# Optimization experiments

Measured on AMD Instinct MI355X. Metric: run time of the kernel, lower is better.

The kernel has to match this reference:

```python
import jax, jax.numpy as jnp
import numpy as np

NS = 8  # number of bins (init arg ns)


def setup_inputs() -> dict:
    key = jax.random.key(0)
    x = jax.random.normal(key, (16, 512, 128, 128), dtype=jnp.float32)
    return {"x": x}


def _make_hk(Hc, C, ns, height):
    """Sequential threshold binning: per batch row, scan j and record bin edges.

    Hc: [B, height] exclusive cumulative counts of per-(b,c) argmax rows.
    Returns hks: [B, ns+1] float32 with hks[:,0]=0, hks[:,ns]=height.
    """

    def row_fn(hrow):
        hks0 = jnp.zeros(ns + 1, jnp.float32).at[ns].set(float(height))

        def step(carry, j):
            k, hks = carry
            t = ((k * C) // ns).astype(hrow.dtype)  # int(k*C/ns)
            cond = (k < ns) & (hrow[j] <= t) & (hrow[j + 1] > t)
            hks = hks.at[k].set(jnp.where(cond, j.astype(jnp.float32), hks[k]))
            k = k + cond.astype(k.dtype)
            return (k, hks), None

        # original loop: j in [1, height-2] (breaks when j+1 >= height)
        js = jnp.arange(1, height - 1, dtype=jnp.int32)
        (_, hks), _ = jax.lax.scan(step, (jnp.int32(1), hks0), js)
        return hks

    return jax.vmap(row_fn)(Hc)


def _forward(x, ns):
    B, C, H, W = x.shape
    a = x.reshape(B, C, H * W)
    vmax = jnp.max(a, axis=2, keepdims=True)
    # argmax indicator mask (ties all set to 1, matching a == max)
    I = (a == vmax).astype(x.dtype).reshape(B, C, H, W)
    # per-row counts of argmax positions, summed over channels & width: [B, H]
    rc = I.sum(axis=(1, 3))
    # H[:, i] = sum of I over rows < i  -> exclusive cumulative sum
    Hc = jnp.concatenate(
        [jnp.zeros((B, 1), x.dtype), jnp.cumsum(rc, axis=1)[:, :-1]], axis=1
    )
    hk = _make_hk(Hc, C, ns, H)  # [B, ns+1]
    F = x.sum(axis=(2, 3)) / W  # [B, C]
    hk_sub = hk[:, 1:] - hk[:, :-1]  # [B, ns]
    # F repeated over ns bins, divided by bin widths, flattened: [B, ns*C]
    return (F[:, None, :] / hk_sub[:, :, None]).reshape(B, ns * C)


def reference(x):
    return _forward(x, NS)
```

## Files before the change

### kernel.cpp

```cpp
#include <hip/hip_runtime.h>

#define Bdim 16
#define Cdim 512
#define Hdim 128
#define Wdim 128
#define NS 8

__global__ __launch_bounds__(256) void chan_reduce(const float* __restrict__ x,
                                                   int* __restrict__ rc,
                                                   float* __restrict__ F) {
    const int bid = blockIdx.x;
    const int tid = threadIdx.x;
    const float4* __restrict__ p = (const float4*)(x + ((size_t)bid << 14));

    float4 r[16];
    float tmax = -INFINITY;
    float tsum = 0.f;
#pragma unroll
    for (int i = 0; i < 16; ++i) {
        r[i] = p[i * 256 + tid];
        tsum += (r[i].x + r[i].y) + (r[i].z + r[i].w);
        tmax = fmaxf(tmax, fmaxf(fmaxf(r[i].x, r[i].y), fmaxf(r[i].z, r[i].w)));
    }

#pragma unroll
    for (int off = 32; off > 0; off >>= 1) {
        tsum += __shfl_down(tsum, off, 64);
        tmax = fmaxf(tmax, __shfl_down(tmax, off, 64));
    }

    __shared__ float smax[4], ssum[4];
    const int wave = tid >> 6;
    if ((tid & 63) == 0) { smax[wave] = tmax; ssum[wave] = tsum; }
    __syncthreads();

    const float bmax = fmaxf(fmaxf(smax[0], smax[1]), fmaxf(smax[2], smax[3]));
    if (tid == 0) {
        F[bid] = (ssum[0] + ssum[1] + ssum[2] + ssum[3]) * (1.0f / Wdim);
    }

    const int b = bid >> 9;
    const int rsub = tid >> 5;
#pragma unroll
    for (int i = 0; i < 16; ++i) {
        int cnt = (r[i].x == bmax) + (r[i].y == bmax) +
                  (r[i].z == bmax) + (r[i].w == bmax);
        if (cnt) atomicAdd(&rc[b * Hdim + i * 8 + rsub], cnt);
    }
}

__global__ __launch_bounds__(256) void finalize(const int* __restrict__ rc,
                                                const float* __restrict__ F,
                                                float* __restrict__ out) {
    const int b = blockIdx.x;
    const int tid = threadIdx.x;
    __shared__ int s_rc[Hdim];
    __shared__ int s_Hc[Hdim + 1];
    __shared__ float s_sub[NS];

    if (tid < Hdim) s_rc[tid] = rc[b * Hdim + tid];
    __syncthreads();

    if (tid == 0) {
        s_Hc[0] = 0;
        for (int i = 1; i <= Hdim; ++i) s_Hc[i] = s_Hc[i - 1] + s_rc[i - 1];
        float hks[NS + 1];
        for (int k = 0; k <= NS; ++k) hks[k] = 0.f;
        hks[NS] = (float)Hdim;
        int k = 1;
        for (int j = 1; j <= Hdim - 2; ++j) {
            int t = (k * Cdim) / NS;
            if (k < NS && s_Hc[j] <= t && s_Hc[j + 1] > t) {
                hks[k] = (float)j;
                ++k;
            }
        }
        for (int q = 0; q < NS; ++q) s_sub[q] = hks[q + 1] - hks[q];
    }
    __syncthreads();

    for (int idx = tid; idx < NS * Cdim; idx += 256) {
        int k = idx >> 9;
        int c = idx & (Cdim - 1);
        out[b * (NS * Cdim) + idx] = F[b * Cdim + c] / s_sub[k];
    }
}

extern "C" void kernel_launch(void* const* d_in, const int* in_sizes, int n_in,
                              void* d_out, int out_size, void* d_ws, size_t ws_size,
                              hipStream_t stream) {
    const float* x = (const float*)d_in[0];
    float* out = (float*)d_out;
    int* rc = (int*)d_ws;
    float* F = (float*)((char*)d_ws + Bdim * Hdim * sizeof(int));

    hipMemsetAsync(rc, 0, Bdim * Hdim * sizeof(int), stream);
    chan_reduce<<<Bdim * Cdim, 256, 0, stream>>>(x, rc, F);
    finalize<<<Bdim, 256, 0, stream>>>(rc, F, out);
}
```

Before: 687.5 us.

## Fuse finalize into reduction via last-block-done counter, use nontemporal loads

Merges the finalize kernel into the channel reduction kernel. The last block to finish each batch, detected with an atomic done counter and thread fences, computes the bin edges and writes the output, which removes one kernel launch. Input loads become nontemporal and the sum/max accumulation is split into two independent chains. The change adds a fence and an atomic per block, and the tail work now runs serially inside the last block of each batch.

```diff
diff --git a/kernel.cpp b/kernel.cpp
--- a/kernel.cpp
+++ b/kernel.cpp
@@ -6,22 +6,38 @@
 #define Wdim 128
 #define NS 8
 
-__global__ __launch_bounds__(256) void chan_reduce(const float* __restrict__ x,
-                                                   int* __restrict__ rc,
-                                                   float* __restrict__ F) {
+typedef float fvec4 __attribute__((ext_vector_type(4)));
+
+#define RC_OFF   0
+#define DONE_OFF (Bdim * Hdim)
+#define ZERO_BYTES ((Bdim * Hdim + Bdim) * sizeof(int))
+
+__global__ __launch_bounds__(256) void chan_reduce_fused(const float* __restrict__ x,
+                                                         int* __restrict__ ws_i,
+                                                         float* __restrict__ F,
+                                                         float* __restrict__ out) {
+    int* __restrict__ rc   = ws_i + RC_OFF;
+    int* __restrict__ done = ws_i + DONE_OFF;
+
     const int bid = blockIdx.x;
     const int tid = threadIdx.x;
-    const float4* __restrict__ p = (const float4*)(x + ((size_t)bid << 14));
+    const int b = bid >> 9;
+    const fvec4* __restrict__ p = (const fvec4*)(x + ((size_t)bid << 14));
 
-    float4 r[16];
-    float tmax = -INFINITY;
-    float tsum = 0.f;
+    fvec4 r[16];
+    float tmax0 = -INFINITY, tmax1 = -INFINITY;
+    float tsum0 = 0.f, tsum1 = 0.f;
 #pragma unroll
-    for (int i = 0; i < 16; ++i) {
-        r[i] = p[i * 256 + tid];
-        tsum += (r[i].x + r[i].y) + (r[i].z + r[i].w);
-        tmax = fmaxf(tmax, fmaxf(fmaxf(r[i].x, r[i].y), fmaxf(r[i].z, r[i].w)));
+    for (int i = 0; i < 16; i += 2) {
+        r[i]     = __builtin_nontemporal_load(&p[i * 256 + tid]);
+        r[i + 1] = __builtin_nontemporal_load(&p[(i + 1) * 256 + tid]);
+        tsum0 += (r[i].x + r[i].y) + (r[i].z + r[i].w);
+        tsum1 += (r[i+1].x + r[i+1].y) + (r[i+1].z + r[i+1].w);
+        tmax0 = fmaxf(tmax0, fmaxf(fmaxf(r[i].x, r[i].y), fmaxf(r[i].z, r[i].w)));
+        tmax1 = fmaxf(tmax1, fmaxf(fmaxf(r[i+1].x, r[i+1].y), fmaxf(r[i+1].z, r[i+1].w)));
     }
+    float tsum = tsum0 + tsum1;
+    float tmax = fmaxf(tmax0, tmax1);
 
 #pragma unroll
     for (int off = 32; off > 0; off >>= 1) {
@@ -39,7 +55,6 @@
         F[bid] = (ssum[0] + ssum[1] + ssum[2] + ssum[3]) * (1.0f / Wdim);
     }
 
-    const int b = bid >> 9;
     const int rsub = tid >> 5;
 #pragma unroll
     for (int i = 0; i < 16; ++i) {
@@ -47,23 +62,27 @@
                   (r[i].z == bmax) + (r[i].w == bmax);
         if (cnt) atomicAdd(&rc[b * Hdim + i * 8 + rsub], cnt);
     }
-}
 
-__global__ __launch_bounds__(256) void finalize(const int* __restrict__ rc,
-                                                const float* __restrict__ F,
-                                                float* __restrict__ out) {
-    const int b = blockIdx.x;
-    const int tid = threadIdx.x;
-    __shared__ int s_rc[Hdim];
+    __threadfence();
+    __shared__ int s_last;
+    if (tid == 0) {
+        int prev = atomicAdd(&done[b], 1);
+        s_last = (prev == Cdim - 1);
+    }
+    __syncthreads();
+    if (!s_last) return;
+    __threadfence();
+
     __shared__ int s_Hc[Hdim + 1];
     __shared__ float s_sub[NS];
 
-    if (tid < Hdim) s_rc[tid] = rc[b * Hdim + tid];
+    if (tid < Hdim) s_Hc[tid + 1] = atomicAdd(&rc[b * Hdim + tid], 0);
     __syncthreads();
 
     if (tid == 0) {
+        int acc = 0;
         s_Hc[0] = 0;
-        for (int i = 1; i <= Hdim; ++i) s_Hc[i] = s_Hc[i - 1] + s_rc[i - 1];
+        for (int i = 1; i <= Hdim; ++i) { acc += s_Hc[i]; s_Hc[i] = acc; }
         float hks[NS + 1];
         for (int k = 0; k <= NS; ++k) hks[k] = 0.f;
         hks[NS] = (float)Hdim;
@@ -79,10 +98,11 @@
     }
     __syncthreads();
 
+    const float* Fb = F + b * Cdim;
     for (int idx = tid; idx < NS * Cdim; idx += 256) {
         int k = idx >> 9;
         int c = idx & (Cdim - 1);
-        out[b * (NS * Cdim) + idx] = F[b * Cdim + c] / s_sub[k];
+        out[b * (NS * Cdim) + idx] = Fb[c] / s_sub[k];
     }
 }
 
@@ -91,10 +111,9 @@
                               hipStream_t stream) {
     const float* x = (const float*)d_in[0];
     float* out = (float*)d_out;
-    int* rc = (int*)d_ws;
-    float* F = (float*)((char*)d_ws + Bdim * Hdim * sizeof(int));
+    int* ws_i = (int*)d_ws;
+    float* F = (float*)((char*)d_ws + ZERO_BYTES);
 
-    hipMemsetAsync(rc, 0, Bdim * Hdim * sizeof(int), stream);
-    chan_reduce<<<Bdim * Cdim, 256, 0, stream>>>(x, rc, F);
-    finalize<<<Bdim, 256, 0, stream>>>(rc, F, out);
+    (void)hipMemsetAsync(d_ws, 0, ZERO_BYTES, stream);
+    chan_reduce_fused<<<Bdim * Cdim, 256, 0, stream>>>(x, ws_i, F, out);
 }
```

New measurement: 2.142 ms. 3.12x slower.
